# Optimization experiments

Hardware: AMD Instinct MI355X
Metric: run time of the kernel (lower is better)

The kernel has to match this reference:

```python
import jax, jax.numpy as jnp
import numpy as np

GRID_SIDE = 32          # grid_side
H = 512                 # hidden dim
SEQ = 8192              # sequence length
DX = 1.0                # grid spacing (fixed in __init__)


def setup_inputs() -> dict:
    key = jax.random.key(0)
    ks = jax.random.split(key, 8)
    G = GRID_SIDE * GRID_SIDE
    x = jax.random.normal(ks[0], (SEQ, H), dtype=jnp.float32)
    c = jax.random.normal(ks[1], (G,), dtype=jnp.float32) * 0.1
    kp_diag = jax.random.normal(ks[2], (GRID_SIDE,), dtype=jnp.float32) * 0.1
    k_diag = jax.random.normal(ks[3], (GRID_SIDE,), dtype=jnp.float32) * 0.1
    dt_matrix = jax.random.normal(ks[4], (GRID_SIDE, GRID_SIDE), dtype=jnp.float32) * 0.1
    B = jax.random.normal(ks[5], (G, H), dtype=jnp.float32) * 0.01
    C = jax.random.normal(ks[6], (H, G), dtype=jnp.float32) * 0.01
    D = jax.random.uniform(ks[7], (H,), dtype=jnp.float32) * 0.01
    return dict(x=x, c=c, kp_diag=kp_diag, k_diag=k_diag,
                dt_matrix=dt_matrix, B=B, C=C, D=D)


def _fdtd_forward(x, c, kp_diag, k_diag, dt_matrix, B, C, D):
    gs = GRID_SIDE
    G = gs * gs
    dx = DX
    sp = jax.nn.softplus

    # ---- get_positive_parameters ----
    c_pos = sp(c)
    kp_d = jnp.clip(sp(kp_diag), 1e-4, 0.2)
    k_d = jnp.clip(sp(k_diag), 1e-4, 0.2)
    dt2d = jnp.clip(jnp.exp(dt_matrix), 0.1, 5.0)           # [gs, gs]
    max_c = 0.7 * dx / dt2d
    c_pos = jnp.clip(c_pos.reshape(gs, gs), 0.01, 0.9 * max_c).reshape(-1)
    dt = dt2d.reshape(-1)                                    # [G]

    # ---- input projection ----
    Bu = x @ B.T                                             # [S, G]

    # ---- apply_fdtd: extra softplus+clip on diag params (as in source) ----
    kp_d2 = jnp.clip(sp(kp_d), 1e-4, 0.5)
    k_d2 = jnp.clip(sp(k_d), 1e-4, 0.5)

    # ---- construct_fdtd_eigendecomposition ----
    idx = jnp.arange(0, G, gs + 1)[:gs]
    kp_full = jnp.zeros((G,), dtype=x.dtype).at[idx].set(kp_d2)
    k_full = jnp.zeros((G,), dtype=x.dtype).at[idx].set(k_d2)
    kp_full = jnp.clip(sp(kp_full), 1e-4, 0.5)
    k_full = jnp.clip(sp(k_full), 1e-4, 0.5)
    xi = jnp.pi / (2 * dx)
    dt_s = jnp.clip(dt, 0.1, 5.0)
    d1 = jnp.maximum(1.0 + dt_s * k_full, 0.1)
    d2 = jnp.maximum(1.0 + dt_s * kp_full, 0.1)
    lam1 = 1.0 / d1
    real_part = 0.5 * (1.0 / d2 + 1.0 / d1)
    c_safe = jnp.clip(c_pos, 0.01, 1.0)
    imag_part = jnp.clip(c_safe * dt_s * xi / jnp.sqrt(jnp.maximum(d1 * d2, 1e-6)), -10.0, 10.0)
    lam2 = (real_part + 1j * imag_part).astype(jnp.complex64)
    lam3 = (real_part - 1j * imag_part).astype(jnp.complex64)
    factor = (1j * imag_part / jnp.maximum(jnp.abs(real_part - lam1), 1e-3)).astype(jnp.complex64)

    # ---- modal forcing ----
    scaling = 1.0 / (1.0 + dt * kp_full)                     # [G]
    sBu = (Bu * scaling).astype(jnp.complex64)               # [S, G]
    zeros = jnp.zeros_like(sBu)
    F = jnp.concatenate([zeros, sBu, jnp.conjugate(sBu)], axis=1)        # [S, 3G]
    Lambda = jnp.concatenate([lam1.astype(jnp.complex64), lam2, lam3])   # [3G]
    lam_seq = jnp.broadcast_to(Lambda, F.shape)

    # ---- diagonal linear recurrence via associative scan ----
    def binop(left, right):
        A1, b1 = left
        A2, b2 = right
        return (A2 * A1, A2 * b1 + b2)

    _, b_all = jax.lax.associative_scan(binop, (lam_seq, F))  # [S, 3G]

    m1 = b_all[:, :G]
    m2 = b_all[:, G:2 * G]
    m3 = b_all[:, 2 * G:]
    p = jnp.real(m2 + m3)                                     # pressure field [S, G]
    # ox = oy = real(m1 + factor*m2 + conj(factor)*m3) (unused in output)

    # ---- output projection + skip (y = C p + D x) ----
    out = p @ C.T + x * D                                     # [S, H]
    return out


def reference(x, c, kp_diag, k_diag, dt_matrix, B, C, D):
    return _fdtd_forward(x, c, kp_diag, k_diag, dt_matrix, B, C, D)
```

## Files before the change

kernel.cpp:

```cpp
#include <hip/hip_runtime.h>
#include <math.h>


#define SEQ 8192
#define HDIM 512
#define GS 32
#define G 1024
#define CHUNK 64
#define NCH (SEQ / CHUNK)

typedef unsigned short u16;
typedef unsigned int u32;
typedef __attribute__((ext_vector_type(8))) short short8;
typedef __attribute__((ext_vector_type(4))) float f32x4;

#define AS1 __attribute__((address_space(1)))
#define AS3 __attribute__((address_space(3)))

__device__ __forceinline__ float softplusf(float z) {
    return fmaxf(z, 0.0f) + log1pf(expf(-fabsf(z)));
}
__device__ __forceinline__ float clipf(float v, float lo, float hi) {
    return fminf(fmaxf(v, lo), hi);
}
__device__ __forceinline__ void split2(float f, u16& h, u16& l) {
    u32 b = __float_as_uint(f);
    u32 hb = (b + 0x8000u) & 0xffff0000u;
    h = (u16)(hb >> 16);
    float r = f - __uint_as_float(hb);
    l = (u16)((__float_as_uint(r) + 0x8000u) >> 16);
}
template<int N> __device__ __forceinline__ void waitv() {
    if constexpr (N == 0)      asm volatile("s_waitcnt vmcnt(0)" ::: "memory");
    else if constexpr (N == 6) asm volatile("s_waitcnt vmcnt(6)" ::: "memory");
    else if constexpr (N == 8) asm volatile("s_waitcnt vmcnt(8)" ::: "memory");
}

__global__ void params_kernel(const float* __restrict__ c,
                              const float* __restrict__ kp_diag,
                              const float* __restrict__ k_diag,
                              const float* __restrict__ dt_matrix,
                              float* __restrict__ lam_re, float* __restrict__ lam_im,
                              float* __restrict__ scal,
                              float* __restrict__ lamC_re, float* __restrict__ lamC_im) {
    int g = blockIdx.x * blockDim.x + threadIdx.x;
    if (g >= G) return;
    float dt = clipf(expf(dt_matrix[g]), 0.1f, 5.0f);
    float max_c = 0.7f / dt;
    float c_pos = clipf(softplusf(c[g]), 0.01f, 0.9f * max_c);

    float kp_base = 0.0f, k_base = 0.0f;
    if (g % (GS + 1) == 0) {
        int d = g / (GS + 1);
        float kp_d = clipf(softplusf(kp_diag[d]), 1e-4f, 0.2f);
        kp_base = clipf(softplusf(kp_d), 1e-4f, 0.5f);
        float k_d = clipf(softplusf(k_diag[d]), 1e-4f, 0.2f);
        k_base = clipf(softplusf(k_d), 1e-4f, 0.5f);
    }
    float kp_full = clipf(softplusf(kp_base), 1e-4f, 0.5f);
    float k_full  = clipf(softplusf(k_base),  1e-4f, 0.5f);

    float d1 = fmaxf(1.0f + dt * k_full, 0.1f);
    float d2 = fmaxf(1.0f + dt * kp_full, 0.1f);
    float real_part = 0.5f * (1.0f / d2 + 1.0f / d1);
    float c_safe = clipf(c_pos, 0.01f, 1.0f);
    const float xi = 1.5707963267948966f;
    float imag_part = clipf(c_safe * dt * xi / sqrtf(fmaxf(d1 * d2, 1e-6f)), -10.0f, 10.0f);

    lam_re[g] = real_part;
    lam_im[g] = imag_part;
    scal[g] = 1.0f / (1.0f + dt * kp_full);

    float ar = real_part, ai = imag_part;
#pragma unroll
    for (int s = 0; s < 6; ++s) {
        float nr = ar * ar - ai * ai;
        float ni = 2.0f * ar * ai;
        ar = nr; ai = ni;
    }
    lamC_re[g] = ar; lamC_im[g] = ai;
}

#define N4X (SEQ * HDIM / 4)
#define N4B (G * HDIM / 4)
#define N4C (HDIM * G / 4)
__global__ __launch_bounds__(256)
void split_all(const float* __restrict__ x,  u16* __restrict__ xh,  u16* __restrict__ xl,
               const float* __restrict__ B,  u16* __restrict__ Bh,  u16* __restrict__ Bl,
               const float* __restrict__ Cm, u16* __restrict__ Ch,  u16* __restrict__ Cl) {
    int stride = gridDim.x * 256;
    for (int i = blockIdx.x * 256 + threadIdx.x; i < N4X + N4B + N4C; i += stride) {
        const float* in; u16* hi; u16* lo; int j = i;
        if (j < N4X) { in = x; hi = xh; lo = xl; }
        else if (j < N4X + N4B) { j -= N4X; in = B; hi = Bh; lo = Bl; }
        else { j -= N4X + N4B; in = Cm; hi = Ch; lo = Cl; }
        float4 v = ((const float4*)in)[j];
        ushort4 h, l;
        split2(v.x, h.x, l.x); split2(v.y, h.y, l.y);
        split2(v.z, h.z, l.z); split2(v.w, h.w, l.w);
        ((ushort4*)hi)[j] = h;
        ((ushort4*)lo)[j] = l;
    }
}

template<int BM, int BN, int WM, int WN, bool SCALE_EPI, int MINW>
__global__ __launch_bounds__(256, MINW)
void gemm_split(const u16* __restrict__ Ah, const u16* __restrict__ Al,
                const u16* __restrict__ Bh, const u16* __restrict__ Bl,
                float* __restrict__ Cout, int M, int N, int K,
                const float* __restrict__ scal,
                const float* __restrict__ xres, const float* __restrict__ Dv) {
    constexpr int MI = WM / 16, NI = WN / 16;
    constexpr int ACH = BM / 16, BCH = BN / 16;
    constexpr int oAh = 0, oAl = BM * 32;
    constexpr int oBh = 2 * BM * 32, oBl = 2 * BM * 32 + BN * 32;
    constexpr int BUFS = 2 * BM * 32 + 2 * BN * 32;
    constexpr int LPW = (ACH + BCH) / 2;
    __shared__ __align__(16) u16 sm[2][BUFS];

    const int tid = threadIdx.x;
    const int lane = tid & 63, wid = tid >> 6;
    const int wrow = wid >> 1, wcol = wid & 1;
    const int lr = lane & 15, lg = lane >> 4;

    const int flat = blockIdx.y * gridDim.x + blockIdx.x;
    const int cpx = (gridDim.x * gridDim.y) >> 3;
    const int swz = (flat & 7) * cpx + (flat >> 3);
    const int m0 = (swz / gridDim.x) * BM, n0 = (swz % gridDim.x) * BN;

    const u16* gbs[4]   = {Ah, Al, Bh, Bl};
    const int  nchs[4]  = {ACH, ACH, BCH, BCH};
    const int  row0s[4] = {m0, m0, n0, n0};
    const int  ofss[4]  = {oAh, oAl, oBh, oBl};

    const int srow = lane >> 2;
    const int shp  = lane & 3;

    auto stage = [&](int buf, int kt) {
#pragma unroll
        for (int a = 0; a < 4; ++a) {
            for (int c = wid; c < nchs[a]; c += 4) {
                int r = c * 16 + srow;
                int h = shp ^ ((r >> 1) & 3);
                const u16* gp = gbs[a] + (size_t)(row0s[a] + r) * K + kt + h * 8;
                u16* lp = &sm[buf][ofss[a] + c * 512];
                __builtin_amdgcn_global_load_lds((const AS1 u32*)gp, (AS3 u32*)lp, 16, 0, 0);
            }
        }
    };

    f32x4 acc[MI][NI];
#pragma unroll
    for (int i = 0; i < MI; ++i)
#pragma unroll
        for (int j = 0; j < NI; ++j) acc[i][j] = (f32x4){0.f, 0.f, 0.f, 0.f};

    const int NT = K / 32;
    stage(0, 0);
    for (int t = 0; t < NT; ++t) {
        const int buf = t & 1;
        if (t + 1 < NT) {
            stage(buf ^ 1, (t + 1) * 32);
            waitv<LPW>();
        } else {
            waitv<0>();
        }
        __builtin_amdgcn_sched_barrier(0);
        __builtin_amdgcn_s_barrier();
        __builtin_amdgcn_sched_barrier(0);

        const u16* smc = sm[buf];
        short8 fah[MI], fal[MI], fbh[NI], fbl[NI];
#pragma unroll
        for (int mi = 0; mi < MI; ++mi) {
            int r = wrow * WM + mi * 16 + lr;
            int idx = r * 32 + ((lg ^ ((r >> 1) & 3)) * 8);
            fah[mi] = *(const short8*)&smc[oAh + idx];
            fal[mi] = *(const short8*)&smc[oAl + idx];
        }
#pragma unroll
        for (int ni = 0; ni < NI; ++ni) {
            int r = wcol * WN + ni * 16 + lr;
            int idx = r * 32 + ((lg ^ ((r >> 1) & 3)) * 8);
            fbh[ni] = *(const short8*)&smc[oBh + idx];
            fbl[ni] = *(const short8*)&smc[oBl + idx];
        }
#pragma unroll
        for (int mi = 0; mi < MI; ++mi)
#pragma unroll
            for (int ni = 0; ni < NI; ++ni) {
                acc[mi][ni] = __builtin_amdgcn_mfma_f32_16x16x32_bf16(fah[mi], fbh[ni], acc[mi][ni], 0, 0, 0);
                acc[mi][ni] = __builtin_amdgcn_mfma_f32_16x16x32_bf16(fah[mi], fbl[ni], acc[mi][ni], 0, 0, 0);
                acc[mi][ni] = __builtin_amdgcn_mfma_f32_16x16x32_bf16(fal[mi], fbh[ni], acc[mi][ni], 0, 0, 0);
            }
        __builtin_amdgcn_s_barrier();
    }

#pragma unroll
    for (int mi = 0; mi < MI; ++mi)
#pragma unroll
        for (int ni = 0; ni < NI; ++ni) {
            int col = n0 + wcol * WN + ni * 16 + lr;
            int rbase = m0 + wrow * WM + mi * 16 + lg * 4;
            if constexpr (SCALE_EPI) {
                float s = scal[col];
#pragma unroll
                for (int v = 0; v < 4; ++v)
                    Cout[(size_t)(rbase + v) * N + col] = acc[mi][ni][v] * s;
            } else {
                float dv = Dv[col];
#pragma unroll
                for (int v = 0; v < 4; ++v) {
                    size_t o = (size_t)(rbase + v) * N + col;
                    Cout[o] = fmaf(xres[o], dv, acc[mi][ni][v]);
                }
            }
        }
}

__global__ __launch_bounds__(256)
void scan_carry(const float* __restrict__ sBu,
                const float* __restrict__ lam_re, const float* __restrict__ lam_im,
                float2* __restrict__ carry) {
    int g = blockIdx.x * 256 + threadIdx.x;
    int ch = blockIdx.y;
    const float lr = lam_re[g], li = lam_im[g];
    const float* f = sBu + (size_t)ch * CHUNK * G + g;
    float hr = 0.0f, hi = 0.0f;
    for (int tb = 0; tb < CHUNK / 8; ++tb) {
        float fb[8];
#pragma unroll
        for (int u = 0; u < 8; ++u) fb[u] = f[(size_t)(tb * 8 + u) * G];
#pragma unroll
        for (int u = 0; u < 8; ++u) {
            float nr = fmaf(lr, hr, fmaf(-li, hi, fb[u]));
            float ni = fmaf(lr, hi, li * hr);
            hr = nr; hi = ni;
        }
    }
    carry[(size_t)ch * G + g] = make_float2(hr, hi);
}

__global__ void carry_scan(const float2* __restrict__ carry,
                           const float* __restrict__ lamC_re, const float* __restrict__ lamC_im,
                           float2* __restrict__ carry_in) {
    int g = blockIdx.x * blockDim.x + threadIdx.x;
    if (g >= G) return;
    const float lr = lamC_re[g], li = lamC_im[g];
    float hr = 0.0f, hi = 0.0f;
    for (int cb = 0; cb < NCH; cb += 8) {
        float2 loc[8];
#pragma unroll
        for (int u = 0; u < 8; ++u) loc[u] = carry[(size_t)(cb + u) * G + g];
#pragma unroll
        for (int u = 0; u < 8; ++u) {
            carry_in[(size_t)(cb + u) * G + g] = make_float2(hr, hi);
            float nr = fmaf(lr, hr, -li * hi) + loc[u].x;
            float ni = fmaf(lr, hi, li * hr) + loc[u].y;
            hr = nr; hi = ni;
        }
    }
}

__global__ __launch_bounds__(256)
void scan_emit(const float* __restrict__ sBu, u16* __restrict__ ph, u16* __restrict__ pl,
               const float* __restrict__ lam_re, const float* __restrict__ lam_im,
               const float2* __restrict__ carry_in) {
    int g = blockIdx.x * 256 + threadIdx.x;
    int ch = blockIdx.y;
    const float lr = lam_re[g], li = lam_im[g];
    const float* f = sBu + (size_t)ch * CHUNK * G + g;
    u16* oh = ph + (size_t)ch * CHUNK * G + g;
    u16* ol = pl + (size_t)ch * CHUNK * G + g;
    float2 h0 = carry_in[(size_t)ch * G + g];
    float hr = h0.x, hi = h0.y;
    for (int tb = 0; tb < CHUNK / 8; ++tb) {
        float fb[8];
#pragma unroll
        for (int u = 0; u < 8; ++u) fb[u] = f[(size_t)(tb * 8 + u) * G];
#pragma unroll
        for (int u = 0; u < 8; ++u) {
            float nr = fmaf(lr, hr, fmaf(-li, hi, fb[u]));
            float ni = fmaf(lr, hi, li * hr);
            hr = nr; hi = ni;
            float p = 2.0f * hr;
            u16 hh, ll; split2(p, hh, ll);
            oh[(size_t)(tb * 8 + u) * G] = hh;
            ol[(size_t)(tb * 8 + u) * G] = ll;
        }
    }
}

extern "C" void kernel_launch(void* const* d_in, const int* in_sizes, int n_in,
                              void* d_out, int out_size, void* d_ws, size_t ws_size,
                              hipStream_t stream) {
    const float* x   = (const float*)d_in[0];
    const float* c   = (const float*)d_in[1];
    const float* kp  = (const float*)d_in[2];
    const float* kd  = (const float*)d_in[3];
    const float* dtm = (const float*)d_in[4];
    const float* B   = (const float*)d_in[5];
    const float* Cm  = (const float*)d_in[6];
    const float* D   = (const float*)d_in[7];
    float* out = (float*)d_out;

    char* w = (char*)d_ws;
    float* sBu = (float*)w;              w += (size_t)SEQ * G * 4;
    u16* ph = (u16*)w;                   w += (size_t)SEQ * G * 2;
    u16* pl = (u16*)w;                   w += (size_t)SEQ * G * 2;
    u16* xh = (u16*)w;                   w += (size_t)SEQ * HDIM * 2;
    u16* xl = (u16*)w;                   w += (size_t)SEQ * HDIM * 2;
    u16* Bh_ = (u16*)w;                  w += (size_t)G * HDIM * 2;
    u16* Bl_ = (u16*)w;                  w += (size_t)G * HDIM * 2;
    u16* Ch_ = (u16*)w;                  w += (size_t)HDIM * G * 2;
    u16* Cl_ = (u16*)w;                  w += (size_t)HDIM * G * 2;
    float* lam_re  = (float*)w;          w += G * 4;
    float* lam_im  = (float*)w;          w += G * 4;
    float* scal    = (float*)w;          w += G * 4;
    float* lamC_re = (float*)w;          w += G * 4;
    float* lamC_im = (float*)w;          w += G * 4;
    float2* carry    = (float2*)w;       w += (size_t)NCH * G * 8;
    float2* carry_in = (float2*)w;

    params_kernel<<<dim3(G / 256), 256, 0, stream>>>(c, kp, kd, dtm, lam_re, lam_im,
                                                     scal, lamC_re, lamC_im);
    split_all<<<dim3(2048), 256, 0, stream>>>(x, xh, xl, B, Bh_, Bl_, Cm, Ch_, Cl_);

    gemm_split<128, 128, 64, 64, true, 2>
        <<<dim3(G / 128, SEQ / 128), 256, 0, stream>>>(xh, xl, Bh_, Bl_, sBu,
                                                       SEQ, G, HDIM, scal, nullptr, nullptr);

    scan_carry<<<dim3(G / 256, NCH), 256, 0, stream>>>(sBu, lam_re, lam_im, carry);
    carry_scan<<<dim3(G / 256), 256, 0, stream>>>(carry, lamC_re, lamC_im, carry_in);
    scan_emit<<<dim3(G / 256, NCH), 256, 0, stream>>>(sBu, ph, pl, lam_re, lam_im, carry_in);

    gemm_split<128, 64, 64, 32, false, 3>
        <<<dim3(HDIM / 64, SEQ / 128), 256, 0, stream>>>(ph, pl, Ch_, Cl_, out,
                                                         SEQ, HDIM, G, nullptr, x, D);
}
```

Measured before the change: 182.3 us.

## Fuse chunk-carry scan into input-projection GEMM epilogue via LDS staging

The per-chunk carry computation of the linear recurrence moves into the first GEMM's epilogue. Accumulators are staged in shared memory; half the threads run the 128-step complex recurrence per column to produce chunk carries, while the other half write the scaled tile with float4 stores. Chunk size rises to 128 to match the GEMM row tile, and the carry multiplier becomes lambda^128. This removes a separate kernel launch and one full re-read of sBu, but serialises a 128-step dependency chain inside each GEMM block and makes scan_emit work on longer chunks.

```diff
diff --git a/kernel.cpp b/kernel.cpp
--- a/kernel.cpp
+++ b/kernel.cpp
@@ -6,7 +6,7 @@
 #define HDIM 512
 #define GS 32
 #define G 1024
-#define CHUNK 64
+#define CHUNK 128
 #define NCH (SEQ / CHUNK)
 
 typedef unsigned short u16;
@@ -73,7 +73,7 @@
 
     float ar = real_part, ai = imag_part;
 #pragma unroll
-    for (int s = 0; s < 6; ++s) {
+    for (int s = 0; s < 7; ++s) {
         float nr = ar * ar - ai * ai;
         float ni = 2.0f * ar * ai;
         ar = nr; ai = ni;
@@ -109,7 +109,9 @@
                 const u16* __restrict__ Bh, const u16* __restrict__ Bl,
                 float* __restrict__ Cout, int M, int N, int K,
                 const float* __restrict__ scal,
-                const float* __restrict__ xres, const float* __restrict__ Dv) {
+                const float* __restrict__ xres, const float* __restrict__ Dv,
+                const float* __restrict__ lam_re, const float* __restrict__ lam_im,
+                float2* __restrict__ carry_out) {
     constexpr int MI = WM / 16, NI = WN / 16;
     constexpr int ACH = BM / 16, BCH = BN / 16;
     constexpr int oAh = 0, oAl = BM * 32;
@@ -196,18 +198,54 @@
         __builtin_amdgcn_s_barrier();
     }
 
-#pragma unroll
-    for (int mi = 0; mi < MI; ++mi)
-#pragma unroll
-        for (int ni = 0; ni < NI; ++ni) {
-            int col = n0 + wcol * WN + ni * 16 + lr;
-            int rbase = m0 + wrow * WM + mi * 16 + lg * 4;
-            if constexpr (SCALE_EPI) {
-                float s = scal[col];
+    if constexpr (SCALE_EPI) {
+        float* smf = (float*)&sm[0][0];
+#pragma unroll
+        for (int mi = 0; mi < MI; ++mi)
+#pragma unroll
+            for (int ni = 0; ni < NI; ++ni) {
+                int col = wcol * WN + ni * 16 + lr;
+                int rbase = wrow * WM + mi * 16 + lg * 4;
 #pragma unroll
                 for (int v = 0; v < 4; ++v)
-                    Cout[(size_t)(rbase + v) * N + col] = acc[mi][ni][v] * s;
-            } else {
+                    smf[(rbase + v) * BM + col] = acc[mi][ni][v];
+            }
+        __syncthreads();
+        if (tid < 128) {
+            int col = tid;
+            float s  = scal[n0 + col];
+            float lre = lam_re[n0 + col], lim = lam_im[n0 + col];
+            float hr = 0.0f, hi = 0.0f;
+            for (int b = 0; b < BM / 8; ++b) {
+                float fb[8];
+#pragma unroll
+                for (int u = 0; u < 8; ++u) fb[u] = smf[(b * 8 + u) * BM + col] * s;
+#pragma unroll
+                for (int u = 0; u < 8; ++u) {
+                    float nr = fmaf(lre, hr, fmaf(-lim, hi, fb[u]));
+                    float ni = fmaf(lre, hi, lim * hr);
+                    hr = nr; hi = ni;
+                }
+            }
+            carry_out[(size_t)(m0 >> 7) * N + n0 + col] = make_float2(hr, hi);
+        } else {
+            int t = tid - 128;
+            int c4 = t & 31, rg = t >> 5;
+            float4 s4 = *(const float4*)&scal[n0 + c4 * 4];
+            for (int it = 0; it < BM / 4; ++it) {
+                int r = it * 4 + rg;
+                float4 v4 = *(float4*)&smf[r * BM + c4 * 4];
+                v4.x *= s4.x; v4.y *= s4.y; v4.z *= s4.z; v4.w *= s4.w;
+                *(float4*)&Cout[(size_t)(m0 + r) * N + n0 + c4 * 4] = v4;
+            }
+        }
+    } else {
+#pragma unroll
+        for (int mi = 0; mi < MI; ++mi)
+#pragma unroll
+            for (int ni = 0; ni < NI; ++ni) {
+                int col = n0 + wcol * WN + ni * 16 + lr;
+                int rbase = m0 + wrow * WM + mi * 16 + lg * 4;
                 float dv = Dv[col];
 #pragma unroll
                 for (int v = 0; v < 4; ++v) {
@@ -215,30 +253,7 @@
                     Cout[o] = fmaf(xres[o], dv, acc[mi][ni][v]);
                 }
             }
-        }
-}
-
-__global__ __launch_bounds__(256)
-void scan_carry(const float* __restrict__ sBu,
-                const float* __restrict__ lam_re, const float* __restrict__ lam_im,
-                float2* __restrict__ carry) {
-    int g = blockIdx.x * 256 + threadIdx.x;
-    int ch = blockIdx.y;
-    const float lr = lam_re[g], li = lam_im[g];
-    const float* f = sBu + (size_t)ch * CHUNK * G + g;
-    float hr = 0.0f, hi = 0.0f;
-    for (int tb = 0; tb < CHUNK / 8; ++tb) {
-        float fb[8];
-#pragma unroll
-        for (int u = 0; u < 8; ++u) fb[u] = f[(size_t)(tb * 8 + u) * G];
-#pragma unroll
-        for (int u = 0; u < 8; ++u) {
-            float nr = fmaf(lr, hr, fmaf(-li, hi, fb[u]));
-            float ni = fmaf(lr, hi, li * hr);
-            hr = nr; hi = ni;
-        }
-    }
-    carry[(size_t)ch * G + g] = make_float2(hr, hi);
+    }
 }
 
 __global__ void carry_scan(const float2* __restrict__ carry,
@@ -328,13 +343,14 @@
 
     gemm_split<128, 128, 64, 64, true, 2>
         <<<dim3(G / 128, SEQ / 128), 256, 0, stream>>>(xh, xl, Bh_, Bl_, sBu,
-                                                       SEQ, G, HDIM, scal, nullptr, nullptr);
-
-    scan_carry<<<dim3(G / 256, NCH), 256, 0, stream>>>(sBu, lam_re, lam_im, carry);
+                                                       SEQ, G, HDIM, scal, nullptr, nullptr,
+                                                       lam_re, lam_im, carry);
+
     carry_scan<<<dim3(G / 256), 256, 0, stream>>>(carry, lamC_re, lamC_im, carry_in);
     scan_emit<<<dim3(G / 256, NCH), 256, 0, stream>>>(sBu, ph, pl, lam_re, lam_im, carry_in);
 
     gemm_split<128, 64, 64, 32, false, 3>
         <<<dim3(HDIM / 64, SEQ / 128), 256, 0, stream>>>(ph, pl, Ch_, Cl_, out,
-                                                         SEQ, HDIM, G, nullptr, x, D);
-}
+                                                         SEQ, HDIM, G, nullptr, x, D,
+                                                         nullptr, nullptr, nullptr);
+}
```

Result: faster. 173.1 us (-5.1%).
